# Optimization experiments

Measured on AMD Instinct MI355X. Metric: run time of the kernel, lower is better.

Reference implementation:

```python
import jax, jax.numpy as jnp
import numpy as np

EPS = 1e-16


def setup_inputs() -> dict:
    key = jax.random.key(0)
    ks = jax.random.split(key, 7)
    B, N, C = 4096, 2048, 128  # batch of heads, memory rows, memory cols
    k = jax.random.normal(ks[0], (B, C), dtype=jnp.float32)
    beta = jax.random.normal(ks[1], (B, 1), dtype=jnp.float32)
    g = jax.random.normal(ks[2], (B, 1), dtype=jnp.float32)
    s = jax.random.normal(ks[3], (B, 3), dtype=jnp.float32)
    gamma = jax.random.normal(ks[4], (B, 1), dtype=jnp.float32)
    w_prev = jax.random.uniform(ks[5], (B, N), dtype=jnp.float32)
    w_prev = w_prev / jnp.sum(w_prev, axis=1, keepdims=True)  # valid weighting
    M = jax.random.normal(ks[6], (N, C), dtype=jnp.float32)  # memory matrix
    return {"k": k, "beta": beta, "g": g, "s": s, "gamma": gamma,
            "w_prev": w_prev, "M": M}


def reference(k, beta, g, s, gamma, w_prev, M):
    # head activations
    beta = jax.nn.softplus(beta)            # [B,1] key strength > 0
    g = jax.nn.sigmoid(g)                   # [B,1] interpolation gate
    s = jax.nn.softmax(s, axis=-1)          # [B,3] shift distribution
    gamma = 1.0 + jax.nn.softplus(gamma)    # [B,1] sharpening >= 1

    # content addressing: cosine similarity k vs memory rows
    k_norm = jnp.linalg.norm(k, axis=-1, keepdims=True)          # [B,1]
    m_norm = jnp.linalg.norm(M, axis=-1, keepdims=True)          # [N,1]
    sim = jnp.einsum('bc,nc->bn', k, M) / (k_norm * m_norm.T + EPS)  # [B,N]
    w_c = jax.nn.softmax(beta * sim, axis=-1)                    # [B,N]

    # interpolation with previous weighting
    w_g = g * w_c + (1.0 - g) * w_prev                           # [B,N]

    # circular convolution with 3-tap shift kernel (shifts -1, 0, +1)
    w_tilde = (s[:, 0:1] * jnp.roll(w_g, 1, axis=1)
               + s[:, 1:2] * w_g
               + s[:, 2:3] * jnp.roll(w_g, -1, axis=1))          # [B,N]

    # sharpening
    w_sharp = w_tilde ** gamma
    w = w_sharp / (jnp.sum(w_sharp, axis=1, keepdims=True) + EPS)
    return w
```

## Files before the change

### kernel.cpp

```cpp
#include <hip/hip_runtime.h>
#include <math.h>

#define NN 2048
#define CC 128
#define EPSF 1e-16f

typedef __attribute__((ext_vector_type(8))) short bf16x8;
typedef __attribute__((ext_vector_type(4))) float f32x4;

__device__ __forceinline__ float softplusf(float x) {
  return fmaxf(x, 0.0f) + log1pf(__expf(-fabsf(x)));
}
__device__ __forceinline__ float wave_sum(float v) {
#pragma unroll
  for (int o = 32; o; o >>= 1) v += __shfl_xor(v, o, 64);
  return v;
}

union U8 { uint u[4]; bf16x8 v; };

__device__ __forceinline__ void split8s(const float* f, bf16x8& hi, bf16x8& lo) {
  U8 H, L;
#pragma unroll
  for (int i = 0; i < 4; ++i) {
    float f0 = f[2 * i], f1 = f[2 * i + 1];
    uint u0 = __float_as_uint(f0), u1 = __float_as_uint(f1);
    uint m0 = u0 & 0xffff0000u, m1 = u1 & 0xffff0000u;
    float r0 = f0 - __uint_as_float(m0);
    float r1 = f1 - __uint_as_float(m1);
    H.u[i] = (u0 >> 16) | m1;
    L.u[i] = (__float_as_uint(r0) >> 16) | (__float_as_uint(r1) & 0xffff0000u);
  }
  hi = H.v;
  lo = L.v;
}

__device__ __forceinline__ void gl2lds16(const void* gsrc, void* ldst) {
  __builtin_amdgcn_global_load_lds(
      (const __attribute__((address_space(1))) void*)gsrc,
      (__attribute__((address_space(3))) void*)ldst, 16, 0, 0);
}

__global__ __launch_bounds__(256) void ntm_prep_kernel(
    const float* __restrict__ kptr, const float* __restrict__ beta_,
    const float* __restrict__ g_, const float* __restrict__ s_,
    const float* __restrict__ gamma_, const float* __restrict__ M,
    bf16x8* __restrict__ Mhf, bf16x8* __restrict__ Mlf,
    bf16x8* __restrict__ Khf, bf16x8* __restrict__ Klf,
    float* __restrict__ gvv, float* __restrict__ gmv,
    float* __restrict__ s0a, float* __restrict__ s1a,
    float* __restrict__ s2a) {
  const int bid = blockIdx.x;
  const int t = threadIdx.x;
  if (bid < 96) {
    const int lane = t & 63;
    const int wv = t >> 6;
    const int l15 = lane & 15;
    const int lg = lane >> 4;
    const bool isM = bid < 32;
    const int grp = (isM ? bid : bid - 32) * 4 + wv;
    const int nrow = isM ? ((grp >> 3) * 128 + 8 * l15 + (grp & 7))
                         : (grp * 16 + l15);
    const float* src = (isM ? M : kptr) + nrow * CC + lg * 8;
    bf16x8* dh = (isM ? Mhf : Khf) + (grp * 4) * 64 + lane;
    bf16x8* dl = (isM ? Mlf : Klf) + (grp * 4) * 64 + lane;

    float f[4][8];
    float sq = 0.f;
#pragma unroll
    for (int ks = 0; ks < 4; ++ks) {
      float4 a0 = *(const float4*)(src + ks * 32);
      float4 a1 = *(const float4*)(src + ks * 32 + 4);
      f[ks][0] = a0.x; f[ks][1] = a0.y; f[ks][2] = a0.z; f[ks][3] = a0.w;
      f[ks][4] = a1.x; f[ks][5] = a1.y; f[ks][6] = a1.z; f[ks][7] = a1.w;
#pragma unroll
      for (int j = 0; j < 8; ++j) sq += f[ks][j] * f[ks][j];
    }
    sq += __shfl_xor(sq, 16, 64);
    sq += __shfl_xor(sq, 32, 64);
    const float nrm = sqrtf(sq);
    const float scale = isM ? (1.0f / nrm) : (softplusf(beta_[nrow]) / nrm);
#pragma unroll
    for (int ks = 0; ks < 4; ++ks) {
#pragma unroll
      for (int j = 0; j < 8; ++j) f[ks][j] *= scale;
      bf16x8 h, l;
      split8s(f[ks], h, l);
      dh[ks * 64] = h;
      dl[ks * 64] = l;
    }
  } else {
    const int r = (bid - 96) * 256 + t;
    gvv[r] = 1.0f / (1.0f + __expf(-g_[r]));
    gmv[r] = 1.0f + softplusf(gamma_[r]);
    float sh0 = s_[3 * r], sh1 = s_[3 * r + 1], sh2 = s_[3 * r + 2];
    float shm = fmaxf(sh0, fmaxf(sh1, sh2));
    float e0 = __expf(sh0 - shm), e1 = __expf(sh1 - shm), e2 = __expf(sh2 - shm);
    float sden = 1.0f / (e0 + e1 + e2);
    s0a[r] = e0 * sden;
    s1a[r] = e1 * sden;
    s2a[r] = e2 * sden;
  }
}

__global__ __launch_bounds__(1024) void ntm_main_kernel(
    const float* __restrict__ w_prev, const bf16x8* __restrict__ Mhf,
    const bf16x8* __restrict__ Mlf, const bf16x8* __restrict__ Khf,
    const bf16x8* __restrict__ Klf, const float* __restrict__ gvv,
    const float* __restrict__ gmv, const float* __restrict__ s0a,
    const float* __restrict__ s1a, const float* __restrict__ s2a,
    float* __restrict__ out) {
  __shared__ __align__(16) char smem[131072];
  char* Areg = smem;
  float (*eQ)[2048] = (float(*)[2048])smem;

  const int t = threadIdx.x;
  const int lane = t & 63;
  const int w = __builtin_amdgcn_readfirstlane(t >> 6);
  const int l15 = lane & 15;
  const int lg = lane >> 4;
  const int bg = blockIdx.x;
  const int b0 = bg * 16;

  if (w == 0) {
#pragma unroll
    for (int ks = 0; ks < 4; ++ks) {
      gl2lds16(&Khf[(bg * 4 + ks) * 64 + lane], Areg + (ks * 2 + 0) * 1024);
      gl2lds16(&Klf[(bg * 4 + ks) * 64 + lane], Areg + (ks * 2 + 1) * 1024);
    }
  }
  char* myB = smem + 8192 + w * 6144;
  const int gw = 8 * w;
#define STAGEB(c)                                                          \
  {                                                                        \
    const int ks_ = (c) >> 3, tt_ = (c)&7;                                 \
    gl2lds16(&Mhf[((gw + tt_) * 4 + ks_) * 64 + lane],                     \
             myB + ((c) % 3) * 2048);                                      \
    gl2lds16(&Mlf[((gw + tt_) * 4 + ks_) * 64 + lane],                     \
             myB + ((c) % 3) * 2048 + 1024);                               \
  }
  STAGEB(0);
  STAGEB(1);
  STAGEB(2);
  __syncthreads();

  f32x4 accT[8];
#pragma unroll
  for (int tt = 0; tt < 8; ++tt) accT[tt] = (f32x4){0.f, 0.f, 0.f, 0.f};

  bf16x8 ah, al;
#pragma unroll
  for (int c = 0; c < 32; ++c) {
    if ((c & 7) == 0) {
      const int ks_ = c >> 3;
      ah = *(const bf16x8*)(Areg + (ks_ * 2 + 0) * 1024 + lane * 16);
      al = *(const bf16x8*)(Areg + (ks_ * 2 + 1) * 1024 + lane * 16);
    }
    if (c <= 29) {
      asm volatile("s_waitcnt vmcnt(4)" ::: "memory");
    } else if (c == 30) {
      asm volatile("s_waitcnt vmcnt(2)" ::: "memory");
    } else {
      asm volatile("s_waitcnt vmcnt(0)" ::: "memory");
    }
    bf16x8 bh = *(const bf16x8*)(myB + (c % 3) * 2048 + lane * 16);
    bf16x8 bl = *(const bf16x8*)(myB + (c % 3) * 2048 + 1024 + lane * 16);
    asm volatile("s_waitcnt lgkmcnt(0)" ::: "memory");
    if (c + 3 < 32) STAGEB(c + 3);
    const int tt = c & 7;
    __builtin_amdgcn_s_setprio(1);
    accT[tt] = __builtin_amdgcn_mfma_f32_16x16x32_bf16(ah, bh, accT[tt], 0, 0, 0);
    accT[tt] = __builtin_amdgcn_mfma_f32_16x16x32_bf16(al, bh, accT[tt], 0, 0, 0);
    accT[tt] = __builtin_amdgcn_mfma_f32_16x16x32_bf16(ah, bl, accT[tt], 0, 0, 0);
    __builtin_amdgcn_s_setprio(0);
  }
#undef STAGEB

  const int ncol0 = 128 * w + 8 * l15;
#pragma unroll
  for (int q = 0; q < 4; ++q) {
#pragma unroll
    for (int tt = 0; tt < 8; ++tt) {
      accT[tt][q] = __expf(accT[tt][q]);
    }
  }

  __syncthreads();

#pragma unroll
  for (int q = 0; q < 4; ++q) {
    *(float4*)&eQ[lg * 4 + q][ncol0] =
        (float4){accT[0][q], accT[1][q], accT[2][q], accT[3][q]};
    *(float4*)&eQ[lg * 4 + q][ncol0 + 4] =
        (float4){accT[4][q], accT[5][q], accT[6][q], accT[7][q]};
  }
  __syncthreads();

  float4 v[8];
#pragma unroll
  for (int b = 0; b < 8; ++b)
    v[b] = *(const float4*)&eQ[w][256 * b + 4 * lane];

  const int row = b0 + w;
  const int lanem1 = (lane + 63) & 63;
  const int lanep1 = (lane + 1) & 63;

  float lsum = 0.f;
#pragma unroll
  for (int b = 0; b < 8; ++b)
    lsum += (v[b].x + v[b].y) + (v[b].z + v[b].w);
  const float tot = wave_sum(lsum);

  const float gv = gvv[row];
  const float ge = gv / tot;
  const float om = 1.0f - gv;
  const float sh0 = s0a[row], sh1 = s1a[row], sh2 = s2a[row];
  const float gammav = gmv[row];

  const float4* w_prev4 = (const float4*)w_prev;
  const size_t rf4 = (size_t)row * (NN / 4) + lane;
#pragma unroll
  for (int b = 0; b < 8; ++b) {
    float4 w4 = w_prev4[rf4 + 64 * b];
    v[b].x = ge * v[b].x + om * w4.x;
    v[b].y = ge * v[b].y + om * w4.y;
    v[b].z = ge * v[b].z + om * w4.z;
    v[b].w = ge * v[b].w + om * w4.w;
  }

  float pm[8], np[8];
#pragma unroll
  for (int b = 0; b < 8; ++b) {
    pm[b] = __shfl(v[b].w, lanem1, 64);
    np[b] = __shfl(v[b].x, lanep1, 64);
  }
  float sp = 0.f;
#pragma unroll
  for (int b = 0; b < 8; ++b) {
    const float pv0 = (lane == 0) ? pm[(b + 7) & 7] : pm[b];
    const float nx3 = (lane == 63) ? np[(b + 1) & 7] : np[b];
    const float w0 = v[b].x, w1 = v[b].y, w2 = v[b].z, w3 = v[b].w;
    float t0 = sh0 * pv0 + sh1 * w0 + sh2 * w1;
    float t1 = sh0 * w0 + sh1 * w1 + sh2 * w2;
    float t2 = sh0 * w1 + sh1 * w2 + sh2 * w3;
    float t3 = sh0 * w2 + sh1 * w3 + sh2 * nx3;
    float p0 = __expf(gammav * __logf(t0));
    float p1 = __expf(gammav * __logf(t1));
    float p2 = __expf(gammav * __logf(t2));
    float p3 = __expf(gammav * __logf(t3));
    v[b].x = p0;
    v[b].y = p1;
    v[b].z = p2;
    v[b].w = p3;
    sp += (p0 + p1) + (p2 + p3);
  }
  const float spt = wave_sum(sp);
  const float pinv = 1.0f / (spt + EPSF);

  float4* out4 = (float4*)out;
#pragma unroll
  for (int b = 0; b < 8; ++b) {
    float4 o;
    o.x = v[b].x * pinv;
    o.y = v[b].y * pinv;
    o.z = v[b].z * pinv;
    o.w = v[b].w * pinv;
    out4[rf4 + 64 * b] = o;
  }
}

union U8F { uint u[4]; bf16x8 v; };
__device__ __forceinline__ void split8f(float4 a, float4 b, bf16x8& hi,
                                        bf16x8& lo, float& sq) {
  float f[8] = {a.x, a.y, a.z, a.w, b.x, b.y, b.z, b.w};
  U8F H, L;
#pragma unroll
  for (int i = 0; i < 4; ++i) {
    float f0 = f[2 * i], f1 = f[2 * i + 1];
    sq += f0 * f0;
    sq += f1 * f1;
    uint u0 = __float_as_uint(f0), u1 = __float_as_uint(f1);
    uint m0 = u0 & 0xffff0000u, m1 = u1 & 0xffff0000u;
    float r0 = f0 - __uint_as_float(m0);
    float r1 = f1 - __uint_as_float(m1);
    H.u[i] = (u0 >> 16) | m1;
    L.u[i] = (__float_as_uint(r0) >> 16) | (__float_as_uint(r1) & 0xffff0000u);
  }
  hi = H.v;
  lo = L.v;
}

__global__ __launch_bounds__(1024) void ntm_main_fallback(
    const float* __restrict__ kptr, const float* __restrict__ beta_,
    const float* __restrict__ g_, const float* __restrict__ s_,
    const float* __restrict__ gamma_, const float* __restrict__ w_prev,
    const float* __restrict__ Mptr, float* __restrict__ out) {
  __shared__ float red[16][16];
  __shared__ float edges[16][16][2];
  const int t = threadIdx.x;
  const int lane = t & 63;
  const int w = __builtin_amdgcn_readfirstlane(t >> 6);
  const int l15 = lane & 15;
  const int lg = lane >> 4;
  const int b0 = blockIdx.x * 16;

  const float* kr = kptr + (b0 + l15) * CC + lg * 8;
  bf16x8 ah[4], al[4];
  float ksq = 0.f;
#pragma unroll
  for (int ks = 0; ks < 4; ++ks) {
    float4 a0 = *(const float4*)(kr + ks * 32);
    float4 a1 = *(const float4*)(kr + ks * 32 + 4);
    split8f(a0, a1, ah[ks], al[ks], ksq);
  }
  ksq += __shfl_xor(ksq, 16, 64);
  ksq += __shfl_xor(ksq, 32, 64);
  const float ikn_own = 1.0f / sqrtf(ksq);

  f32x4 accT[8];
  float imn[8];
#pragma unroll
  for (int tt = 0; tt < 8; ++tt) {
    const int n0t = 128 * w + 16 * tt;
    const float* mr = Mptr + (size_t)(n0t + l15) * CC + lg * 8;
    f32x4 acc = {0.f, 0.f, 0.f, 0.f};
    float msq = 0.f;
#pragma unroll
    for (int ks = 0; ks < 4; ++ks) {
      float4 m0 = *(const float4*)(mr + ks * 32);
      float4 m1 = *(const float4*)(mr + ks * 32 + 4);
      bf16x8 bh, bl;
      split8f(m0, m1, bh, bl, msq);
      acc = __builtin_amdgcn_mfma_f32_16x16x32_bf16(ah[ks], bh, acc, 0, 0, 0);
      acc = __builtin_amdgcn_mfma_f32_16x16x32_bf16(al[ks], bh, acc, 0, 0, 0);
      acc = __builtin_amdgcn_mfma_f32_16x16x32_bf16(ah[ks], bl, acc, 0, 0, 0);
    }
    msq += __shfl_xor(msq, 16, 64);
    msq += __shfl_xor(msq, 32, 64);
    imn[tt] = 1.0f / sqrtf(msq);
    accT[tt] = acc;
  }

#pragma unroll
  for (int q = 0; q < 4; ++q) {
    const int rr = lg * 4 + q;
    const float zb = softplusf(beta_[b0 + rr]) * __shfl(ikn_own, rr, 64);
    float rs = 0.f;
#pragma unroll
    for (int tt = 0; tt < 8; ++tt) {
      float e = __expf(accT[tt][q] * imn[tt] * zb);
      accT[tt][q] = e;
      rs += e;
    }
    rs += __shfl_xor(rs, 1, 64);
    rs += __shfl_xor(rs, 2, 64);
    rs += __shfl_xor(rs, 4, 64);
    rs += __shfl_xor(rs, 8, 64);
    if (l15 == 0) red[rr][w] = rs;
  }
  __syncthreads();

#pragma unroll
  for (int q = 0; q < 4; ++q) {
    const int rr = lg * 4 + q;
    float4 p0 = *(const float4*)&red[rr][0];
    float4 p1 = *(const float4*)&red[rr][4];
    float4 p2 = *(const float4*)&red[rr][8];
    float4 p3 = *(const float4*)&red[rr][12];
    float tot = (p0.x + p0.y + p0.z + p0.w) + (p1.x + p1.y + p1.z + p1.w) +
                (p2.x + p2.y + p2.z + p2.w) + (p3.x + p3.y + p3.z + p3.w);
    const float gv = 1.0f / (1.0f + __expf(-g_[b0 + rr]));
    const float ge = gv / tot;
    const float om = 1.0f - gv;
    const size_t rbase = (size_t)(b0 + rr) * NN + 128 * w + l15;
#pragma unroll
    for (int tt = 0; tt < 8; ++tt) {
      float wpv = w_prev[rbase + 16 * tt];
      accT[tt][q] = ge * accT[tt][q] + om * wpv;
    }
    if (l15 == 0) edges[rr][w][0] = accT[0][q];
    if (l15 == 15) edges[rr][w][1] = accT[7][q];
  }
  __syncthreads();

  const int tm = (lane & 48) | ((lane + 15) & 15);
  const int tp = (lane & 48) | ((lane + 1) & 15);
#pragma unroll
  for (int q = 0; q < 4; ++q) {
    const int rr = lg * 4 + q;
    float sh0 = s_[3 * (b0 + rr)];
    float sh1 = s_[3 * (b0 + rr) + 1];
    float sh2 = s_[3 * (b0 + rr) + 2];
    float shm = fmaxf(sh0, fmaxf(sh1, sh2));
    float e0 = __expf(sh0 - shm), e1 = __expf(sh1 - shm), e2 = __expf(sh2 - shm);
    float sden = 1.0f / (e0 + e1 + e2);
    sh0 = e0 * sden; sh1 = e1 * sden; sh2 = e2 * sden;
    const float gammav = 1.0f + softplusf(gamma_[b0 + rr]);
    const float eL = edges[rr][(w + 15) & 15][1];
    const float eR = edges[rr][(w + 1) & 15][0];
    float sm[8], sp[8];
#pragma unroll
    for (int tt = 0; tt < 8; ++tt) {
      sm[tt] = __shfl(accT[tt][q], tm, 64);
      sp[tt] = __shfl(accT[tt][q], tp, 64);
    }
    float rs = 0.f;
#pragma unroll
    for (int tt = 0; tt < 8; ++tt) {
      float pv = (l15 == 0) ? ((tt == 0) ? eL : sm[tt - 1]) : sm[tt];
      float nx = (l15 == 15) ? ((tt == 7) ? eR : sp[tt + 1]) : sp[tt];
      float wt = sh0 * pv + sh1 * accT[tt][q] + sh2 * nx;
      float p = __expf(gammav * __logf(wt));
      accT[tt][q] = p;
      rs += p;
    }
    rs += __shfl_xor(rs, 1, 64);
    rs += __shfl_xor(rs, 2, 64);
    rs += __shfl_xor(rs, 4, 64);
    rs += __shfl_xor(rs, 8, 64);
    if (l15 == 0) red[rr][w] = rs;
  }
  __syncthreads();

#pragma unroll
  for (int q = 0; q < 4; ++q) {
    const int rr = lg * 4 + q;
    float4 p0 = *(const float4*)&red[rr][0];
    float4 p1 = *(const float4*)&red[rr][4];
    float4 p2 = *(const float4*)&red[rr][8];
    float4 p3 = *(const float4*)&red[rr][12];
    float tot = (p0.x + p0.y + p0.z + p0.w) + (p1.x + p1.y + p1.z + p1.w) +
                (p2.x + p2.y + p2.z + p2.w) + (p3.x + p3.y + p3.z + p3.w);
    const float pinv = 1.0f / (tot + EPSF);
    const size_t rbase = (size_t)(b0 + rr) * NN + 128 * w + l15;
#pragma unroll
    for (int tt = 0; tt < 8; ++tt) {
      out[rbase + 16 * tt] = accT[tt][q] * pinv;
    }
  }
}

extern "C" void kernel_launch(void* const* d_in, const int* in_sizes, int n_in,
                              void* d_out, int out_size, void* d_ws, size_t ws_size,
                              hipStream_t stream) {
  const float* k = (const float*)d_in[0];
  const float* beta = (const float*)d_in[1];
  const float* g = (const float*)d_in[2];
  const float* s = (const float*)d_in[3];
  const float* gamma = (const float*)d_in[4];
  const float* w_prev = (const float*)d_in[5];
  const float* M = (const float*)d_in[6];
  float* out = (float*)d_out;

  char* ws = (char*)d_ws;
  bf16x8* Mhf = (bf16x8*)(ws + 0);
  bf16x8* Mlf = (bf16x8*)(ws + 524288);
  bf16x8* Khf = (bf16x8*)(ws + 1048576);
  bf16x8* Klf = (bf16x8*)(ws + 2097152);
  float* gvv = (float*)(ws + 3145728);
  float* gmv = gvv + 4096;
  float* s0a = gmv + 4096;
  float* s1a = s0a + 4096;
  float* s2a = s1a + 4096;
  const size_t need = 3145728 + 5 * 4096 * 4;

  if (ws_size >= need) {
    ntm_prep_kernel<<<112, 256, 0, stream>>>(k, beta, g, s, gamma, M, Mhf, Mlf,
                                             Khf, Klf, gvv, gmv, s0a, s1a, s2a);
    ntm_main_kernel<<<256, 1024, 0, stream>>>(w_prev, Mhf, Mlf, Khf, Klf, gvv,
                                              gmv, s0a, s1a, s2a, out);
  } else {
    ntm_main_fallback<<<256, 1024, 0, stream>>>(k, beta, g, s, gamma, w_prev,
                                                M, out);
  }
}
```

Measured before the change: 40.17 us.

## Split fused GEMM+softmax kernel into GEMM kernel and separate finish kernel

The fused main kernel is split into a GEMM kernel and a finish kernel. The GEMM kernel runs on 512 blocks, each covering half of the memory columns, and writes exp(scores) plus per-block partial row sums to a workspace. The finish kernel then reads them back to do interpolation, shift, sharpening and normalisation with 4 rows per 256-thread block. This gives the GEMM more parallelism and smaller LDS use, at the cost of writing and re-reading a 32 MB intermediate in global memory and one extra kernel launch.

```diff
diff --git a/kernel.cpp b/kernel.cpp
--- a/kernel.cpp
+++ b/kernel.cpp
@@ -56,11 +56,11 @@
     const int lane = t & 63;
     const int wv = t >> 6;
     const int l15 = lane & 15;
-    const int lg = lane >> 4;
     const bool isM = bid < 32;
     const int grp = (isM ? bid : bid - 32) * 4 + wv;
     const int nrow = isM ? ((grp >> 3) * 128 + 8 * l15 + (grp & 7))
                          : (grp * 16 + l15);
+    const int lg = lane >> 4;
     const float* src = (isM ? M : kptr) + nrow * CC + lg * 8;
     bf16x8* dh = (isM ? Mhf : Khf) + (grp * 4) * 64 + lane;
     bf16x8* dl = (isM ? Mlf : Klf) + (grp * 4) * 64 + lane;
@@ -103,113 +103,103 @@
   }
 }
 
-__global__ __launch_bounds__(1024) void ntm_main_kernel(
-    const float* __restrict__ w_prev, const bf16x8* __restrict__ Mhf,
-    const bf16x8* __restrict__ Mlf, const bf16x8* __restrict__ Khf,
-    const bf16x8* __restrict__ Klf, const float* __restrict__ gvv,
-    const float* __restrict__ gmv, const float* __restrict__ s0a,
-    const float* __restrict__ s1a, const float* __restrict__ s2a,
-    float* __restrict__ out) {
-  __shared__ __align__(16) char smem[131072];
-  char* Areg = smem;
-  float (*eQ)[2048] = (float(*)[2048])smem;
-
+__global__ __launch_bounds__(1024) void ntm_gemm_kernel(
+    const bf16x8* __restrict__ Mhf, const bf16x8* __restrict__ Mlf,
+    const bf16x8* __restrict__ Khf, const bf16x8* __restrict__ Klf,
+    float* __restrict__ ews, float* __restrict__ psum) {
+  __shared__ __align__(16) char smem[73728];
   const int t = threadIdx.x;
   const int lane = t & 63;
   const int w = __builtin_amdgcn_readfirstlane(t >> 6);
   const int l15 = lane & 15;
   const int lg = lane >> 4;
-  const int bg = blockIdx.x;
-  const int b0 = bg * 16;
-
+  const int kg = blockIdx.x >> 1;
+  const int h = blockIdx.x & 1;
+  const int b0 = kg * 16;
+
+  char* Areg = smem;
   if (w == 0) {
 #pragma unroll
     for (int ks = 0; ks < 4; ++ks) {
-      gl2lds16(&Khf[(bg * 4 + ks) * 64 + lane], Areg + (ks * 2 + 0) * 1024);
-      gl2lds16(&Klf[(bg * 4 + ks) * 64 + lane], Areg + (ks * 2 + 1) * 1024);
-    }
-  }
-  char* myB = smem + 8192 + w * 6144;
-  const int gw = 8 * w;
+      gl2lds16(&Khf[(kg * 4 + ks) * 64 + lane], Areg + (ks * 2 + 0) * 1024);
+      gl2lds16(&Klf[(kg * 4 + ks) * 64 + lane], Areg + (ks * 2 + 1) * 1024);
+    }
+  }
+  char* myB = smem + 8192 + w * 4096;
+  const int gbase = h * 64 + 4 * w;
 #define STAGEB(c)                                                          \
   {                                                                        \
-    const int ks_ = (c) >> 3, tt_ = (c)&7;                                 \
-    gl2lds16(&Mhf[((gw + tt_) * 4 + ks_) * 64 + lane],                     \
-             myB + ((c) % 3) * 2048);                                      \
-    gl2lds16(&Mlf[((gw + tt_) * 4 + ks_) * 64 + lane],                     \
-             myB + ((c) % 3) * 2048 + 1024);                               \
+    const int ks_ = (c) >> 2, j_ = (c)&3;                                  \
+    gl2lds16(&Mhf[((gbase + j_) * 4 + ks_) * 64 + lane],                   \
+             myB + ((c)&1) * 2048);                                        \
+    gl2lds16(&Mlf[((gbase + j_) * 4 + ks_) * 64 + lane],                   \
+             myB + ((c)&1) * 2048 + 1024);                                 \
   }
   STAGEB(0);
   STAGEB(1);
-  STAGEB(2);
   __syncthreads();
 
-  f32x4 accT[8];
-#pragma unroll
-  for (int tt = 0; tt < 8; ++tt) accT[tt] = (f32x4){0.f, 0.f, 0.f, 0.f};
+  f32x4 accT[4];
+#pragma unroll
+  for (int j = 0; j < 4; ++j) accT[j] = (f32x4){0.f, 0.f, 0.f, 0.f};
 
   bf16x8 ah, al;
 #pragma unroll
-  for (int c = 0; c < 32; ++c) {
-    if ((c & 7) == 0) {
-      const int ks_ = c >> 3;
+  for (int c = 0; c < 16; ++c) {
+    if ((c & 3) == 0) {
+      const int ks_ = c >> 2;
       ah = *(const bf16x8*)(Areg + (ks_ * 2 + 0) * 1024 + lane * 16);
       al = *(const bf16x8*)(Areg + (ks_ * 2 + 1) * 1024 + lane * 16);
     }
-    if (c <= 29) {
-      asm volatile("s_waitcnt vmcnt(4)" ::: "memory");
-    } else if (c == 30) {
+    if (c < 15) {
       asm volatile("s_waitcnt vmcnt(2)" ::: "memory");
     } else {
       asm volatile("s_waitcnt vmcnt(0)" ::: "memory");
     }
-    bf16x8 bh = *(const bf16x8*)(myB + (c % 3) * 2048 + lane * 16);
-    bf16x8 bl = *(const bf16x8*)(myB + (c % 3) * 2048 + 1024 + lane * 16);
+    bf16x8 bh = *(const bf16x8*)(myB + (c & 1) * 2048 + lane * 16);
+    bf16x8 bl = *(const bf16x8*)(myB + (c & 1) * 2048 + 1024 + lane * 16);
     asm volatile("s_waitcnt lgkmcnt(0)" ::: "memory");
-    if (c + 3 < 32) STAGEB(c + 3);
-    const int tt = c & 7;
-    __builtin_amdgcn_s_setprio(1);
-    accT[tt] = __builtin_amdgcn_mfma_f32_16x16x32_bf16(ah, bh, accT[tt], 0, 0, 0);
-    accT[tt] = __builtin_amdgcn_mfma_f32_16x16x32_bf16(al, bh, accT[tt], 0, 0, 0);
-    accT[tt] = __builtin_amdgcn_mfma_f32_16x16x32_bf16(ah, bl, accT[tt], 0, 0, 0);
-    __builtin_amdgcn_s_setprio(0);
+    if (c + 2 < 16) STAGEB(c + 2);
+    const int j = c & 3;
+    accT[j] = __builtin_amdgcn_mfma_f32_16x16x32_bf16(ah, bh, accT[j], 0, 0, 0);
+    accT[j] = __builtin_amdgcn_mfma_f32_16x16x32_bf16(al, bh, accT[j], 0, 0, 0);
+    accT[j] = __builtin_amdgcn_mfma_f32_16x16x32_bf16(ah, bl, accT[j], 0, 0, 0);
   }
 #undef STAGEB
 
-  const int ncol0 = 128 * w + 8 * l15;
+  const int nbase = (8 * h + (w >> 1)) * 128 + 8 * l15 + 4 * (w & 1);
 #pragma unroll
   for (int q = 0; q < 4; ++q) {
-#pragma unroll
-    for (int tt = 0; tt < 8; ++tt) {
-      accT[tt][q] = __expf(accT[tt][q]);
-    }
-  }
-
-  __syncthreads();
-
-#pragma unroll
-  for (int q = 0; q < 4; ++q) {
-    *(float4*)&eQ[lg * 4 + q][ncol0] =
-        (float4){accT[0][q], accT[1][q], accT[2][q], accT[3][q]};
-    *(float4*)&eQ[lg * 4 + q][ncol0 + 4] =
-        (float4){accT[4][q], accT[5][q], accT[6][q], accT[7][q]};
-  }
-  __syncthreads();
-
-  float4 v[8];
-#pragma unroll
-  for (int b = 0; b < 8; ++b)
-    v[b] = *(const float4*)&eQ[w][256 * b + 4 * lane];
-
-  const int row = b0 + w;
+    const int row = b0 + lg * 4 + q;
+    float e0 = __expf(accT[0][q]);
+    float e1 = __expf(accT[1][q]);
+    float e2 = __expf(accT[2][q]);
+    float e3 = __expf(accT[3][q]);
+    *(float4*)&ews[(size_t)row * NN + nbase] = (float4){e0, e1, e2, e3};
+    float rs = (e0 + e1) + (e2 + e3);
+    rs += __shfl_xor(rs, 1, 64);
+    rs += __shfl_xor(rs, 2, 64);
+    rs += __shfl_xor(rs, 4, 64);
+    rs += __shfl_xor(rs, 8, 64);
+    if (l15 == 0) psum[(size_t)row * 32 + h * 16 + w] = rs;
+  }
+}
+
+__global__ __launch_bounds__(256) void ntm_finish_kernel(
+    const float* __restrict__ ews, const float* __restrict__ psum,
+    const float* __restrict__ w_prev, const float* __restrict__ gvv,
+    const float* __restrict__ gmv, const float* __restrict__ s0a,
+    const float* __restrict__ s1a, const float* __restrict__ s2a,
+    float* __restrict__ out) {
+  const int t = threadIdx.x;
+  const int lane = t & 63;
+  const int wv = __builtin_amdgcn_readfirstlane(t >> 6);
+  const int row = blockIdx.x * 4 + wv;
   const int lanem1 = (lane + 63) & 63;
   const int lanep1 = (lane + 1) & 63;
 
-  float lsum = 0.f;
-#pragma unroll
-  for (int b = 0; b < 8; ++b)
-    lsum += (v[b].x + v[b].y) + (v[b].z + v[b].w);
-  const float tot = wave_sum(lsum);
+  float pl = (lane < 32) ? psum[(size_t)row * 32 + lane] : 0.f;
+  const float tot = wave_sum(pl);
 
   const float gv = gvv[row];
   const float ge = gv / tot;
@@ -217,15 +207,19 @@
   const float sh0 = s0a[row], sh1 = s1a[row], sh2 = s2a[row];
   const float gammav = gmv[row];
 
+  const float4* ews4 = (const float4*)ews;
   const float4* w_prev4 = (const float4*)w_prev;
   const size_t rf4 = (size_t)row * (NN / 4) + lane;
+
+  float4 v[8];
 #pragma unroll
   for (int b = 0; b < 8; ++b) {
+    float4 e4 = ews4[rf4 + 64 * b];
     float4 w4 = w_prev4[rf4 + 64 * b];
-    v[b].x = ge * v[b].x + om * w4.x;
-    v[b].y = ge * v[b].y + om * w4.y;
-    v[b].z = ge * v[b].z + om * w4.z;
-    v[b].w = ge * v[b].w + om * w4.w;
+    v[b].x = ge * e4.x + om * w4.x;
+    v[b].y = ge * e4.y + om * w4.y;
+    v[b].z = ge * e4.z + om * w4.z;
+    v[b].w = ge * e4.w + om * w4.w;
   }
 
   float pm[8], np[8];
@@ -269,11 +263,10 @@
   }
 }
 
-union U8F { uint u[4]; bf16x8 v; };
 __device__ __forceinline__ void split8f(float4 a, float4 b, bf16x8& hi,
                                         bf16x8& lo, float& sq) {
   float f[8] = {a.x, a.y, a.z, a.w, b.x, b.y, b.z, b.w};
-  U8F H, L;
+  U8 H, L;
 #pragma unroll
   for (int i = 0; i < 4; ++i) {
     float f0 = f[2 * i], f1 = f[2 * i + 1];
@@ -462,13 +455,16 @@
   float* s0a = gmv + 4096;
   float* s1a = s0a + 4096;
   float* s2a = s1a + 4096;
-  const size_t need = 3145728 + 5 * 4096 * 4;
+  float* ews = (float*)(ws + (4 << 20));
+  float* psum = (float*)(ws + (36 << 20));
+  const size_t need = (36 << 20) + 4096 * 32 * 4;
 
   if (ws_size >= need) {
     ntm_prep_kernel<<<112, 256, 0, stream>>>(k, beta, g, s, gamma, M, Mhf, Mlf,
                                              Khf, Klf, gvv, gmv, s0a, s1a, s2a);
-    ntm_main_kernel<<<256, 1024, 0, stream>>>(w_prev, Mhf, Mlf, Khf, Klf, gvv,
-                                              gmv, s0a, s1a, s2a, out);
+    ntm_gemm_kernel<<<512, 1024, 0, stream>>>(Mhf, Mlf, Khf, Klf, ews, psum);
+    ntm_finish_kernel<<<1024, 256, 0, stream>>>(ews, psum, w_prev, gvv, gmv,
+                                                s0a, s1a, s2a, out);
   } else {
     ntm_main_fallback<<<256, 1024, 0, stream>>>(k, beta, g, s, gamma, w_prev,
                                                 M, out);
```

After: 50.16 us. +24.9%, slower.
